# Kernel tuning notes

Measured on AMD Instinct MI355X. Metric: run time of the kernel, lower is better.

Reference implementation:

```python
import jax, jax.numpy as jnp
import numpy as np

VOCAB = 32000; DIM = 512; NL = 6; B = 2; L = 1024
DI = 2 * DIM      # d_inner (expand=2)
DS = 16           # d_state
DC = 4            # d_conv
DR = DIM // 16    # dt_rank = ceil(512/16) = 32


def setup_inputs() -> dict:
    key = jax.random.key(0)
    ks = jax.random.split(key, 10)
    s = 0.02
    tokens = jax.random.randint(ks[0], (B, L), 0, VOCAB)
    pos_emb = jax.random.normal(ks[1], (1, L, DIM)) * s
    embed = jax.random.normal(ks[2], (VOCAB, DIM)) * s
    lm_w = jax.random.normal(ks[3], (VOCAB, DIM)) * s
    lm_b = jnp.zeros((VOCAB,), jnp.float32)
    in_proj_w = jax.random.normal(ks[4], (NL, 2 * DI, DIM)) * s
    conv_w = jax.random.normal(ks[5], (NL, DI, DC)) * s
    conv_b = jnp.zeros((NL, DI), jnp.float32)
    x_proj_w = jax.random.normal(ks[6], (NL, DR + 2 * DS, DI)) * s
    dt_proj_w = jax.random.normal(ks[7], (NL, DI, DR)) * s
    dt_proj_b = jnp.broadcast_to(jnp.log(jnp.expm1(jnp.float32(0.01))), (NL, DI)).astype(jnp.float32)
    A_log = jnp.log(jnp.broadcast_to(jnp.arange(1, DS + 1, dtype=jnp.float32), (NL, DI, DS)))
    Dp = jnp.ones((NL, DI), jnp.float32)
    out_w = jax.random.normal(ks[8], (NL, DIM, DI)) * s
    ln_g = jnp.ones((NL, DIM), jnp.float32)
    ln_b = jnp.zeros((NL, DIM), jnp.float32)
    return dict(tokens=tokens, pos_emb=pos_emb, embed=embed, lm_w=lm_w, lm_b=lm_b,
                in_proj_w=in_proj_w, conv_w=conv_w, conv_b=conv_b, x_proj_w=x_proj_w,
                dt_proj_w=dt_proj_w, dt_proj_b=dt_proj_b, A_log=A_log, Dp=Dp,
                out_w=out_w, ln_g=ln_g, ln_b=ln_b)


def silu(x):
    return x * jax.nn.sigmoid(x)


def layernorm(x, g, b, eps=1e-5):
    mu = jnp.mean(x, -1, keepdims=True)
    var = jnp.var(x, -1, keepdims=True)
    return (x - mu) * jax.lax.rsqrt(var + eps) * g + b


def causal_dwconv(x, w, b):
    # x: (B,L,DI), w: (DI,DC) depthwise, left-pad causal
    xp = jnp.pad(x, ((0, 0), (DC - 1, 0), (0, 0)))
    y = b
    for k in range(DC):
        y = y + w[:, k] * xp[:, k:k + x.shape[1], :]
    return y


def selective_scan(u, dt, A, Bm, Cm, Dp):
    # u,dt: (B,L,DI); A: (DI,DS); Bm,Cm: (B,L,DS)
    dA = jnp.exp(dt[..., None] * A)                       # (B,L,DI,DS)
    dBu = dt[..., None] * Bm[:, :, None, :] * u[..., None]
    h0 = jnp.zeros((u.shape[0], DI, DS), u.dtype)

    def step(h, inp):
        dA_t, dBu_t, C_t = inp
        h = dA_t * h + dBu_t
        y = jnp.einsum('bdn,bn->bd', h, C_t)
        return h, y

    _, ys = jax.lax.scan(step, h0, (dA.transpose(1, 0, 2, 3),
                                    dBu.transpose(1, 0, 2, 3),
                                    Cm.transpose(1, 0, 2)))
    return ys.transpose(1, 0, 2) + u * Dp


def mamba_block(x, in_w, cw, cb, xp_w, dtw, dtb, A_log, Dp, ow):
    xz = jnp.einsum('bld,ed->ble', x, in_w)               # (B,L,2*DI)
    xc, z = jnp.split(xz, 2, axis=-1)
    xc = silu(causal_dwconv(xc, cw, cb))
    x_dbl = jnp.einsum('bld,ed->ble', xc, xp_w)           # (B,L,DR+2*DS)
    dt, Bm, Cm = jnp.split(x_dbl, [DR, DR + DS], axis=-1)
    dt = jax.nn.softplus(jnp.einsum('blr,dr->bld', dt, dtw) + dtb)
    A = -jnp.exp(A_log)
    y = selective_scan(xc, dt, A, Bm, Cm, Dp)
    y = y * silu(z)
    return jnp.einsum('bld,ed->ble', y, ow)


def reference(tokens, pos_emb, embed, lm_w, lm_b, in_proj_w, conv_w, conv_b,
              x_proj_w, dt_proj_w, dt_proj_b, A_log, Dp, out_w, ln_g, ln_b):
    x = embed[tokens] + pos_emb[:, :tokens.shape[1]]
    for i in range(NL):
        res = x
        x = mamba_block(x, in_proj_w[i], conv_w[i], conv_b[i], x_proj_w[i],
                        dt_proj_w[i], dt_proj_b[i], A_log[i], Dp[i], out_w[i])
        x = layernorm(x + res, ln_g[i], ln_b[i])
    return jnp.einsum('bld,vd->blv', x, lm_w) + lm_b
```

## Files before the change

kernel.cpp:

```cpp
#include <hip/hip_runtime.h>
#include <hip/hip_bf16.h>
#include <math.h>

#define BB 2
#define LL 1024
#define DIM 512
#define NL 6
#define DI 1024
#define DS 16
#define DC 4
#define DR 32
#define VOCAB 32000
#define M_ROWS (BB * LL)
#define CCH 64
#define CHLEN (LL / CCH)
#define KSPLIT 8

typedef unsigned short u16;
typedef __attribute__((ext_vector_type(8))) short bf16x8;
typedef __attribute__((ext_vector_type(4))) float f32x4;

__device__ __forceinline__ u16 f2bf(float f) {
    unsigned u = __float_as_uint(f);
    u += 0x7FFF + ((u >> 16) & 1);
    return (u16)(u >> 16);
}
#define SWZ(r, c) ((c) ^ (((r) >> 1) & 3))

__global__ __launch_bounds__(256) void cast_all(const float* __restrict__ lm,
                                                const float* __restrict__ inw,
                                                const float* __restrict__ ow,
                                                const float* __restrict__ xp,
                                                u16* __restrict__ lmb,
                                                u16* __restrict__ inb,
                                                u16* __restrict__ owb_,
                                                u16* __restrict__ xpb) {
    int idx = blockIdx.x * 256 + threadIdx.x;
    const float* src; u16* dst; int off;
    if (idx < 2048000)      { src = lm;  dst = lmb;  off = idx; }
    else if (idx < 2834432) { src = inw; dst = inb;  off = idx - 2048000; }
    else if (idx < 3227648) { src = ow;  dst = owb_; off = idx - 2834432; }
    else                    { src = xp;  dst = xpb;  off = idx - 3227648; }
    float4 v0 = ((const float4*)src)[off * 2];
    float4 v1 = ((const float4*)src)[off * 2 + 1];
    union { u16 h[8]; int4 v; } r;
    r.h[0] = f2bf(v0.x); r.h[1] = f2bf(v0.y); r.h[2] = f2bf(v0.z); r.h[3] = f2bf(v0.w);
    r.h[4] = f2bf(v1.x); r.h[5] = f2bf(v1.y); r.h[6] = f2bf(v1.z); r.h[7] = f2bf(v1.w);
    ((int4*)dst)[off] = r.v;
}

__global__ __launch_bounds__(256) void embed_kernel(const int* __restrict__ tok,
                                                    const float* __restrict__ pos,
                                                    const float* __restrict__ emb,
                                                    float* __restrict__ x,
                                                    u16* __restrict__ xb) {
    int idx = blockIdx.x * 256 + threadIdx.x;
    int d = idx & (DIM - 1);
    int l = (idx >> 9) & (LL - 1);
    int b = idx >> 19;
    int t = tok[b * LL + l];
    float v = emb[(size_t)t * DIM + d] + pos[l * DIM + d];
    x[idx] = v;
    xb[idx] = f2bf(v);
}

__global__ __launch_bounds__(256) void gemm_bf16(const u16* __restrict__ A,
                                                 const u16* __restrict__ W,
                                                 const float* __restrict__ bias,
                                                 float* __restrict__ C,
                                                 int M, int N, int K,
                                                 int lda, int ldw) {
    __shared__ __align__(16) u16 As[2 * 4096];
    __shared__ __align__(16) u16 Ws[2 * 4096];
    const int t = threadIdx.x;
    const int l = t & 63;
    const int w = t >> 6;
    const int nwg = gridDim.x;
    const int q = nwg >> 3, r8 = nwg & 7;
    const int xcd = blockIdx.x & 7, rank = blockIdx.x >> 3;
    const int wgid = (xcd < r8 ? xcd * (q + 1) : r8 * (q + 1) + (xcd - r8) * q) + rank;
    const int Mb = M >> 7;
    const int bm = (wgid % Mb) * 128;
    const int bn = (wgid / Mb) * 128;
    const int wm = (w >> 1) * 64;
    const int wn = (w & 1) * 64;

    f32x4 acc[4][4] = {};
    const int nt = K >> 5;

    auto STAGE = [&](int bufi, int k0) {
#pragma unroll
        for (int p = 0; p < 2; ++p) {
            const int i = (p * 4 + w) * 64 + l;
            const int row = i >> 2;
            const int kq = SWZ(row, i & 3);
            __builtin_amdgcn_global_load_lds(
                (const __attribute__((address_space(1))) unsigned int*)
                    (A + (size_t)(bm + row) * lda + k0 + kq * 8),
                (__attribute__((address_space(3))) unsigned int*)
                    (As + bufi * 4096 + (p * 4 + w) * 512),
                16, 0, 0);
            __builtin_amdgcn_global_load_lds(
                (const __attribute__((address_space(1))) unsigned int*)
                    (W + (size_t)(bn + row) * ldw + k0 + kq * 8),
                (__attribute__((address_space(3))) unsigned int*)
                    (Ws + bufi * 4096 + (p * 4 + w) * 512),
                16, 0, 0);
        }
    };
    auto COMPUTE = [&](int bufi) {
        const u16* Ab = As + bufi * 4096;
        const u16* Wb = Ws + bufi * 4096;
#pragma unroll
        for (int mi = 0; mi < 4; ++mi) {
            const int ar = wm + mi * 16 + (l & 15);
            bf16x8 a = *(const bf16x8*)(Ab + ar * 32 + SWZ(ar, l >> 4) * 8);
#pragma unroll
            for (int ni = 0; ni < 4; ++ni) {
                const int wr = wn + ni * 16 + (l & 15);
                bf16x8 b = *(const bf16x8*)(Wb + wr * 32 + SWZ(wr, l >> 4) * 8);
                acc[mi][ni] = __builtin_amdgcn_mfma_f32_16x16x32_bf16(b, a, acc[mi][ni], 0, 0, 0);
            }
        }
    };

    STAGE(0, 0);
    for (int tt = 0; tt < nt; ++tt) {
        if (tt + 1 < nt) {
            STAGE((tt + 1) & 1, (tt + 1) << 5);
            asm volatile("s_waitcnt vmcnt(4)\ns_barrier" ::: "memory");
        } else {
            asm volatile("s_waitcnt vmcnt(0)\ns_barrier" ::: "memory");
        }
        COMPUTE(tt & 1);
        asm volatile("s_waitcnt lgkmcnt(0)\ns_barrier" ::: "memory");
    }

#pragma unroll
    for (int mi = 0; mi < 4; ++mi) {
        const int row = bm + wm + mi * 16 + (l & 15);
#pragma unroll
        for (int ni = 0; ni < 4; ++ni) {
            const int col = bn + wn + ni * 16 + ((l >> 4) << 2);
            float4 v;
            v.x = acc[mi][ni][0]; v.y = acc[mi][ni][1];
            v.z = acc[mi][ni][2]; v.w = acc[mi][ni][3];
            if (bias != nullptr) {
                float4 b4 = *(const float4*)(bias + col);
                v.x += b4.x; v.y += b4.y; v.z += b4.z; v.w += b4.w;
            }
            *(float4*)(C + (size_t)row * N + col) = v;
        }
    }
}

__global__ __launch_bounds__(256) void gemm_n64(const u16* __restrict__ A,
                                                const u16* __restrict__ W,
                                                float* __restrict__ out,
                                                int lda, int ldw, int ldc,
                                                int KS, int pstride) {
    __shared__ __align__(16) u16 As[2 * 4096];
    __shared__ __align__(16) u16 Ws[2 * 2048];
    const int t = threadIdx.x;
    const int l = t & 63;
    const int w = t >> 6;
    const int kz = blockIdx.x;
    const int bm = blockIdx.y * 128;
    const int bnn = blockIdx.z * 64;
    const int wm = w * 32;

    f32x4 acc[2][4] = {};
    const int nt = KS >> 5;
    const int kbeg = kz * KS;

    auto STAGE = [&](int bufi, int k0) {
#pragma unroll
        for (int p = 0; p < 2; ++p) {
            const int i = p * 256 + w * 64 + l;
            const int row = i >> 2;
            const int kq = SWZ(row, i & 3);
            __builtin_amdgcn_global_load_lds(
                (const __attribute__((address_space(1))) unsigned int*)
                    (A + (size_t)(bm + row) * lda + k0 + kq * 8),
                (__attribute__((address_space(3))) unsigned int*)
                    (As + bufi * 4096 + (p * 256 + w * 64) * 8),
                16, 0, 0);
        }
        {
            const int i = w * 64 + l;
            const int row = i >> 2;
            const int kq = SWZ(row, i & 3);
            __builtin_amdgcn_global_load_lds(
                (const __attribute__((address_space(1))) unsigned int*)
                    (W + (size_t)(bnn + row) * ldw + k0 + kq * 8),
                (__attribute__((address_space(3))) unsigned int*)
                    (Ws + bufi * 2048 + (w * 64) * 8),
                16, 0, 0);
        }
    };
    auto COMPUTE = [&](int bufi) {
        const u16* Ab = As + bufi * 4096;
        const u16* Wb = Ws + bufi * 2048;
#pragma unroll
        for (int mi = 0; mi < 2; ++mi) {
            const int ar = wm + mi * 16 + (l & 15);
            bf16x8 a = *(const bf16x8*)(Ab + ar * 32 + SWZ(ar, l >> 4) * 8);
#pragma unroll
            for (int ni = 0; ni < 4; ++ni) {
                const int wr = ni * 16 + (l & 15);
                bf16x8 b = *(const bf16x8*)(Wb + wr * 32 + SWZ(wr, l >> 4) * 8);
                acc[mi][ni] = __builtin_amdgcn_mfma_f32_16x16x32_bf16(b, a, acc[mi][ni], 0, 0, 0);
            }
        }
    };

    STAGE(0, kbeg);
    for (int tt = 0; tt < nt; ++tt) {
        if (tt + 1 < nt) {
            STAGE((tt + 1) & 1, kbeg + ((tt + 1) << 5));
            asm volatile("s_waitcnt vmcnt(3)\ns_barrier" ::: "memory");
        } else {
            asm volatile("s_waitcnt vmcnt(0)\ns_barrier" ::: "memory");
        }
        COMPUTE(tt & 1);
        asm volatile("s_waitcnt lgkmcnt(0)\ns_barrier" ::: "memory");
    }

    float* op = out + (size_t)kz * pstride;
#pragma unroll
    for (int mi = 0; mi < 2; ++mi) {
        const int row = bm + wm + mi * 16 + (l & 15);
#pragma unroll
        for (int ni = 0; ni < 4; ++ni) {
            const int col = bnn + ni * 16 + ((l >> 4) << 2);
            float4 v;
            v.x = acc[mi][ni][0]; v.y = acc[mi][ni][1];
            v.z = acc[mi][ni][2]; v.w = acc[mi][ni][3];
            *(float4*)(op + (size_t)row * ldc + col) = v;
        }
    }
}

__global__ __launch_bounds__(256) void xdred_dt(const float* __restrict__ Pf,
                                                const float* __restrict__ dtw,
                                                const float* __restrict__ dtb,
                                                float* __restrict__ xd,
                                                float* __restrict__ dt) {
    __shared__ float xds[64];
    const int m = blockIdx.x;
    const int t = threadIdx.x;
    if (t < 64) {
        float s = 0.f;
#pragma unroll
        for (int kz = 0; kz < KSPLIT; ++kz)
            s += Pf[(size_t)kz * (M_ROWS * 64) + m * 64 + t];
        xds[t] = s;
        xd[m * 64 + t] = s;
    }
    __syncthreads();
    const int d0 = t * 4;
    const float4 bv = *(const float4*)(dtb + d0);
    float a0 = bv.x, a1 = bv.y, a2 = bv.z, a3 = bv.w;
    const float* w0p = dtw + (size_t)(d0 + 0) * DR;
    const float* w1p = dtw + (size_t)(d0 + 1) * DR;
    const float* w2p = dtw + (size_t)(d0 + 2) * DR;
    const float* w3p = dtw + (size_t)(d0 + 3) * DR;
#pragma unroll
    for (int k = 0; k < DR; k += 4) {
        float4 xv = *(const float4*)&xds[k];
        float4 w0 = *(const float4*)(w0p + k);
        float4 w1 = *(const float4*)(w1p + k);
        float4 w2 = *(const float4*)(w2p + k);
        float4 w3 = *(const float4*)(w3p + k);
        a0 += w0.x * xv.x + w0.y * xv.y + w0.z * xv.z + w0.w * xv.w;
        a1 += w1.x * xv.x + w1.y * xv.y + w1.z * xv.z + w1.w * xv.w;
        a2 += w2.x * xv.x + w2.y * xv.y + w2.z * xv.z + w2.w * xv.w;
        a3 += w3.x * xv.x + w3.y * xv.y + w3.z * xv.z + w3.w * xv.w;
    }
    a0 = (a0 > 20.f) ? a0 : log1pf(__expf(a0));
    a1 = (a1 > 20.f) ? a1 : log1pf(__expf(a1));
    a2 = (a2 > 20.f) ? a2 : log1pf(__expf(a2));
    a3 = (a3 > 20.f) ? a3 : log1pf(__expf(a3));
    float4 v; v.x = a0; v.y = a1; v.z = a2; v.w = a3;
    *(float4*)(dt + (size_t)m * DI + d0) = v;
}

__global__ __launch_bounds__(256) void conv_silu(const float* __restrict__ xz,
                                                 const float* __restrict__ cw,
                                                 const float* __restrict__ cb,
                                                 float* __restrict__ xc,
                                                 u16* __restrict__ xcb) {
    int idx = blockIdx.x * 256 + threadIdx.x;
    int c = idx & (DI - 1);
    int l = (idx >> 10) & (LL - 1);
    int b = idx >> 20;
    float acc = cb[c];
#pragma unroll
    for (int k = 0; k < DC; ++k) {
        int ll = l + k - (DC - 1);
        if (ll >= 0)
            acc += cw[c * DC + k] * xz[((size_t)(b * LL + ll)) * (2 * DI) + c];
    }
    float v = acc / (1.f + __expf(-acc));
    xc[idx] = v;
    xcb[idx] = f2bf(v);
}

__global__ __launch_bounds__(256) void scan_pass1(const float* __restrict__ xc,
                                                  const float* __restrict__ dt,
                                                  const float* __restrict__ xdbl,
                                                  const float* __restrict__ A_log,
                                                  float* __restrict__ S,
                                                  float* __restrict__ Q) {
    const int d = blockIdx.x * 256 + threadIdx.x;
    const int b = blockIdx.y;
    const int c = blockIdx.z;
    float a[DS];
#pragma unroll
    for (int q = 0; q < 4; ++q) {
        float4 al = *(const float4*)(A_log + d * DS + q * 4);
        a[q * 4 + 0] = -__expf(al.x);
        a[q * 4 + 1] = -__expf(al.y);
        a[q * 4 + 2] = -__expf(al.z);
        a[q * 4 + 3] = -__expf(al.w);
    }
    float Qr[DS];
#pragma unroll
    for (int n = 0; n < DS; ++n) Qr[n] = 0.f;
    float Ssum = 0.f;

    const int l0 = c * CHLEN;
    const float* dtp = dt + ((size_t)b * LL + l0) * DI + d;
    const float* up  = xc + ((size_t)b * LL + l0) * DI + d;
    const float* xdp = xdbl + ((size_t)b * LL + l0) * 64 + DR;

    for (int l = 0; l < CHLEN; ++l) {
        float dtv = dtp[(size_t)l * DI];
        float uv  = up[(size_t)l * DI];
        float wv = dtv * uv;
        Ssum += dtv;
#pragma unroll
        for (int q = 0; q < 4; ++q) {
            float4 Bv = *(const float4*)(xdp + l * 64 + q * 4);
            float dA0 = __expf(dtv * a[q * 4 + 0]);
            float dA1 = __expf(dtv * a[q * 4 + 1]);
            float dA2 = __expf(dtv * a[q * 4 + 2]);
            float dA3 = __expf(dtv * a[q * 4 + 3]);
            Qr[q * 4 + 0] = dA0 * Qr[q * 4 + 0] + wv * Bv.x;
            Qr[q * 4 + 1] = dA1 * Qr[q * 4 + 1] + wv * Bv.y;
            Qr[q * 4 + 2] = dA2 * Qr[q * 4 + 2] + wv * Bv.z;
            Qr[q * 4 + 3] = dA3 * Qr[q * 4 + 3] + wv * Bv.w;
        }
    }
    S[((size_t)b * CCH + c) * DI + d] = Ssum;
    float* Qp = Q + (((size_t)b * CCH + c) * DI + d) * DS;
#pragma unroll
    for (int q = 0; q < 4; ++q) {
        float4 o;
        o.x = Qr[q * 4 + 0]; o.y = Qr[q * 4 + 1];
        o.z = Qr[q * 4 + 2]; o.w = Qr[q * 4 + 3];
        *(float4*)(Qp + q * 4) = o;
    }
}

__global__ __launch_bounds__(256) void scan_pass2(const float* __restrict__ A_log,
                                                  const float* __restrict__ S,
                                                  float* __restrict__ Q) {
    const int idx = blockIdx.x * 256 + threadIdx.x;
    const int b = idx >> 14;
    const int dn = idx & 16383;
    const int d = dn >> 4;
    const float a = -__expf(A_log[dn]);
    float h = 0.f;
    for (int c = 0; c < CCH; ++c) {
        const size_t soff = ((size_t)b * CCH + c) * DI + d;
        const size_t qoff = ((size_t)b * CCH + c) * (size_t)(DI * DS) + dn;
        float P = __expf(a * S[soff]);
        float qv = Q[qoff];
        Q[qoff] = h;
        h = P * h + qv;
    }
}

__global__ __launch_bounds__(256) void scan_pass3(const float* __restrict__ xc,
                                                  const float* __restrict__ dt,
                                                  const float* __restrict__ xdbl,
                                                  const float* __restrict__ xz,
                                                  const float* __restrict__ A_log,
                                                  const float* __restrict__ Dpp,
                                                  const float* __restrict__ Q,
                                                  u16* __restrict__ y) {
    const int d = blockIdx.x * 256 + threadIdx.x;
    const int b = blockIdx.y;
    const int c = blockIdx.z;
    float a[DS];
#pragma unroll
    for (int q = 0; q < 4; ++q) {
        float4 al = *(const float4*)(A_log + d * DS + q * 4);
        a[q * 4 + 0] = -__expf(al.x);
        a[q * 4 + 1] = -__expf(al.y);
        a[q * 4 + 2] = -__expf(al.z);
        a[q * 4 + 3] = -__expf(al.w);
    }
    float h[DS];
    const float* Qp = Q + (((size_t)b * CCH + c) * DI + d) * DS;
#pragma unroll
    for (int q = 0; q < 4; ++q) {
        float4 hv = *(const float4*)(Qp + q * 4);
        h[q * 4 + 0] = hv.x; h[q * 4 + 1] = hv.y;
        h[q * 4 + 2] = hv.z; h[q * 4 + 3] = hv.w;
    }
    const float dp = Dpp[d];

    const int l0 = c * CHLEN;
    const float* dtp = dt + ((size_t)b * LL + l0) * DI + d;
    const float* up  = xc + ((size_t)b * LL + l0) * DI + d;
    const float* xdp = xdbl + ((size_t)b * LL + l0) * 64 + DR;
    const float* zp  = xz + ((size_t)b * LL + l0) * (2 * DI) + DI + d;
    u16* yp = y + ((size_t)b * LL + l0) * DI + d;

    for (int l = 0; l < CHLEN; ++l) {
        float dtv = dtp[(size_t)l * DI];
        float uv  = up[(size_t)l * DI];
        float wv = dtv * uv;
        float p = 0.f;
#pragma unroll
        for (int q = 0; q < 4; ++q) {
            float4 Bv = *(const float4*)(xdp + l * 64 + q * 4);
            float4 Cv = *(const float4*)(xdp + l * 64 + 16 + q * 4);
            float dA0 = __expf(dtv * a[q * 4 + 0]);
            float dA1 = __expf(dtv * a[q * 4 + 1]);
            float dA2 = __expf(dtv * a[q * 4 + 2]);
            float dA3 = __expf(dtv * a[q * 4 + 3]);
            h[q * 4 + 0] = dA0 * h[q * 4 + 0] + wv * Bv.x;
            h[q * 4 + 1] = dA1 * h[q * 4 + 1] + wv * Bv.y;
            h[q * 4 + 2] = dA2 * h[q * 4 + 2] + wv * Bv.z;
            h[q * 4 + 3] = dA3 * h[q * 4 + 3] + wv * Bv.w;
            p += h[q * 4 + 0] * Cv.x + h[q * 4 + 1] * Cv.y +
                 h[q * 4 + 2] * Cv.z + h[q * 4 + 3] * Cv.w;
        }
        float zv = zp[(size_t)l * (2 * DI)];
        float g = zv / (1.f + __expf(-zv));
        yp[(size_t)l * DI] = f2bf((p + uv * dp) * g);
    }
}

__global__ __launch_bounds__(256) void add_ln(const float* __restrict__ o,
                                              float* __restrict__ x,
                                              const float* __restrict__ g,
                                              const float* __restrict__ b,
                                              u16* __restrict__ xb) {
    int m = blockIdx.x;
    int t = threadIdx.x;
    const float* xr = x + (size_t)m * DIM;
    const float* orr = o + (size_t)m * DIM;
    float v0 = xr[t] + orr[t];
    float v1 = xr[t + 256] + orr[t + 256];
    float s = v0 + v1;
    float ss = v0 * v0 + v1 * v1;
#pragma unroll
    for (int off = 32; off > 0; off >>= 1) {
        s += __shfl_down(s, off, 64);
        ss += __shfl_down(ss, off, 64);
    }
    __shared__ float sb[4], ssb[4];
    int w = t >> 6;
    if ((t & 63) == 0) { sb[w] = s; ssb[w] = ss; }
    __syncthreads();
    float stot = sb[0] + sb[1] + sb[2] + sb[3];
    float sstot = ssb[0] + ssb[1] + ssb[2] + ssb[3];
    float mean = stot * (1.f / DIM);
    float var = sstot * (1.f / DIM) - mean * mean;
    float rs = rsqrtf(var + 1e-5f);
    float* xw = x + (size_t)m * DIM;
    float o0 = (v0 - mean) * rs * g[t] + b[t];
    float o1 = (v1 - mean) * rs * g[t + 256] + b[t + 256];
    xw[t] = o0;
    xw[t + 256] = o1;
    xb[(size_t)m * DIM + t] = f2bf(o0);
    xb[(size_t)m * DIM + t + 256] = f2bf(o1);
}

extern "C" void kernel_launch(void* const* d_in, const int* in_sizes, int n_in,
                              void* d_out, int out_size, void* d_ws, size_t ws_size,
                              hipStream_t stream) {
    const int*   tokens = (const int*)d_in[0];
    const float* pos    = (const float*)d_in[1];
    const float* emb    = (const float*)d_in[2];
    const float* lm_w   = (const float*)d_in[3];
    const float* lm_b   = (const float*)d_in[4];
    const float* in_w   = (const float*)d_in[5];
    const float* cw     = (const float*)d_in[6];
    const float* cb     = (const float*)d_in[7];
    const float* xpw    = (const float*)d_in[8];
    const float* dtw    = (const float*)d_in[9];
    const float* dtb    = (const float*)d_in[10];
    const float* A_log  = (const float*)d_in[11];
    const float* Dpp    = (const float*)d_in[12];
    const float* ow     = (const float*)d_in[13];
    const float* lng    = (const float*)d_in[14];
    const float* lnb    = (const float*)d_in[15];
    float* out = (float*)d_out;

    float* ws = (float*)d_ws;
    float* x    = ws;
    float* xz   = x + 1048576;
    float* xc   = xz + 4194304;
    float* xd   = xc + 2097152;
    float* dt   = xd + 131072;
    float* o    = dt + 2097152;
    float* S    = o + 1048576;
    float* Qb   = S + 131072;
    float* Pf   = Qb + 2097152;
    u16* xb     = (u16*)(Pf + 1048576);
    u16* yb     = xb + 1048576;
    u16* xcb    = yb + 2097152;
    u16* lm_wb  = xcb + 2097152;
    u16* in_wb  = lm_wb + 16384000;
    u16* owb    = in_wb + 6291456;
    u16* xpwb   = owb + 3145728;

    cast_all<<<12800, 256, 0, stream>>>(lm_w, in_w, ow, xpw,
                                        lm_wb, in_wb, owb, xpwb);

    embed_kernel<<<M_ROWS * DIM / 256, 256, 0, stream>>>(tokens, pos, emb, x, xb);

    for (int i = 0; i < NL; ++i) {
        gemm_bf16<<<(2048 / 128) * (M_ROWS / 128), 256, 0, stream>>>(
            xb, in_wb + (size_t)i * 2048 * 512, nullptr, xz,
            M_ROWS, 2048, 512, 512, 512);
        conv_silu<<<M_ROWS * DI / 256, 256, 0, stream>>>(
            xz, cw + (size_t)i * DI * DC, cb + (size_t)i * DI, xc, xcb);
        gemm_n64<<<dim3(KSPLIT, M_ROWS / 128, 1), 256, 0, stream>>>(
            xcb, xpwb + (size_t)i * 64 * 1024, Pf,
            1024, 1024, 64, 1024 / KSPLIT, M_ROWS * 64);
        xdred_dt<<<M_ROWS, 256, 0, stream>>>(
            Pf, dtw + (size_t)i * DI * DR, dtb + (size_t)i * DI, xd, dt);
        scan_pass1<<<dim3(DI / 256, BB, CCH), 256, 0, stream>>>(
            xc, dt, xd, A_log + (size_t)i * DI * DS, S, Qb);
        scan_pass2<<<(BB * DI * DS) / 256, 256, 0, stream>>>(
            A_log + (size_t)i * DI * DS, S, Qb);
        scan_pass3<<<dim3(DI / 256, BB, CCH), 256, 0, stream>>>(
            xc, dt, xd, xz, A_log + (size_t)i * DI * DS, Dpp + (size_t)i * DI, Qb, yb);
        gemm_n64<<<dim3(1, M_ROWS / 128, 512 / 64), 256, 0, stream>>>(
            yb, owb + (size_t)i * 512 * 1024, o,
            1024, 1024, 512, 1024, 0);
        add_ln<<<M_ROWS, 256, 0, stream>>>(
            o, x, lng + (size_t)i * DIM, lnb + (size_t)i * DIM, xb);
    }

    gemm_bf16<<<(VOCAB / 128) * (M_ROWS / 128), 256, 0, stream>>>(
        xb, lm_wb, lm_b, out, M_ROWS, VOCAB, 512, 512, 512);
}
```

Before: 888.4 us.

## Store in_proj output as bf16, split-K out_proj, and shrink scan_pass2 blocks

The in_proj GEMM now runs through gemm_n64 with a bf16 epilogue, so conv_silu and scan_pass3 read xz as bf16 instead of fp32. This halves the traffic for the largest per-layer intermediate. The out_proj GEMM is split four ways along K, giving more blocks in flight, and add_ln sums the four partial results. scan_pass2 moves to 64-thread blocks to launch more blocks. The trade-off is reduced precision on z and the conv input, plus extra partial-sum traffic for out_proj.

```diff
diff --git a/kernel.cpp b/kernel.cpp
--- a/kernel.cpp
+++ b/kernel.cpp
@@ -15,6 +15,7 @@
 #define CCH 64
 #define CHLEN (LL / CCH)
 #define KSPLIT 8
+#define OSPLIT 4
 
 typedef unsigned short u16;
 typedef __attribute__((ext_vector_type(8))) short bf16x8;
@@ -24,6 +25,9 @@
     unsigned u = __float_as_uint(f);
     u += 0x7FFF + ((u >> 16) & 1);
     return (u16)(u >> 16);
+}
+__device__ __forceinline__ float bf2f(u16 h) {
+    return __uint_as_float(((unsigned)h) << 16);
 }
 #define SWZ(r, c) ((c) ^ (((r) >> 1) & 3))
 
@@ -157,6 +161,7 @@
 __global__ __launch_bounds__(256) void gemm_n64(const u16* __restrict__ A,
                                                 const u16* __restrict__ W,
                                                 float* __restrict__ out,
+                                                u16* __restrict__ outb,
                                                 int lda, int ldw, int ldc,
                                                 int KS, int pstride) {
     __shared__ __align__(16) u16 As[2 * 4096];
@@ -226,17 +231,33 @@
         asm volatile("s_waitcnt lgkmcnt(0)\ns_barrier" ::: "memory");
     }
 
-    float* op = out + (size_t)kz * pstride;
-#pragma unroll
-    for (int mi = 0; mi < 2; ++mi) {
-        const int row = bm + wm + mi * 16 + (l & 15);
-#pragma unroll
-        for (int ni = 0; ni < 4; ++ni) {
-            const int col = bnn + ni * 16 + ((l >> 4) << 2);
-            float4 v;
-            v.x = acc[mi][ni][0]; v.y = acc[mi][ni][1];
-            v.z = acc[mi][ni][2]; v.w = acc[mi][ni][3];
-            *(float4*)(op + (size_t)row * ldc + col) = v;
+    if (outb != nullptr) {
+        u16* opb = outb + (size_t)kz * pstride;
+#pragma unroll
+        for (int mi = 0; mi < 2; ++mi) {
+            const int row = bm + wm + mi * 16 + (l & 15);
+#pragma unroll
+            for (int ni = 0; ni < 4; ++ni) {
+                const int col = bnn + ni * 16 + ((l >> 4) << 2);
+                ushort4 v;
+                v.x = f2bf(acc[mi][ni][0]); v.y = f2bf(acc[mi][ni][1]);
+                v.z = f2bf(acc[mi][ni][2]); v.w = f2bf(acc[mi][ni][3]);
+                *(ushort4*)(opb + (size_t)row * ldc + col) = v;
+            }
+        }
+    } else {
+        float* op = out + (size_t)kz * pstride;
+#pragma unroll
+        for (int mi = 0; mi < 2; ++mi) {
+            const int row = bm + wm + mi * 16 + (l & 15);
+#pragma unroll
+            for (int ni = 0; ni < 4; ++ni) {
+                const int col = bnn + ni * 16 + ((l >> 4) << 2);
+                float4 v;
+                v.x = acc[mi][ni][0]; v.y = acc[mi][ni][1];
+                v.z = acc[mi][ni][2]; v.w = acc[mi][ni][3];
+                *(float4*)(op + (size_t)row * ldc + col) = v;
+            }
         }
     }
 }
@@ -285,7 +306,7 @@
     *(float4*)(dt + (size_t)m * DI + d0) = v;
 }
 
-__global__ __launch_bounds__(256) void conv_silu(const float* __restrict__ xz,
+__global__ __launch_bounds__(256) void conv_silu(const u16* __restrict__ xzb,
                                                  const float* __restrict__ cw,
                                                  const float* __restrict__ cb,
                                                  float* __restrict__ xc,
@@ -299,7 +320,7 @@
     for (int k = 0; k < DC; ++k) {
         int ll = l + k - (DC - 1);
         if (ll >= 0)
-            acc += cw[c * DC + k] * xz[((size_t)(b * LL + ll)) * (2 * DI) + c];
+            acc += cw[c * DC + k] * bf2f(xzb[((size_t)(b * LL + ll)) * (2 * DI) + c]);
     }
     float v = acc / (1.f + __expf(-acc));
     xc[idx] = v;
@@ -363,10 +384,10 @@
     }
 }
 
-__global__ __launch_bounds__(256) void scan_pass2(const float* __restrict__ A_log,
-                                                  const float* __restrict__ S,
-                                                  float* __restrict__ Q) {
-    const int idx = blockIdx.x * 256 + threadIdx.x;
+__global__ __launch_bounds__(64) void scan_pass2(const float* __restrict__ A_log,
+                                                 const float* __restrict__ S,
+                                                 float* __restrict__ Q) {
+    const int idx = blockIdx.x * 64 + threadIdx.x;
     const int b = idx >> 14;
     const int dn = idx & 16383;
     const int d = dn >> 4;
@@ -385,7 +406,7 @@
 __global__ __launch_bounds__(256) void scan_pass3(const float* __restrict__ xc,
                                                   const float* __restrict__ dt,
                                                   const float* __restrict__ xdbl,
-                                                  const float* __restrict__ xz,
+                                                  const u16* __restrict__ xzb,
                                                   const float* __restrict__ A_log,
                                                   const float* __restrict__ Dpp,
                                                   const float* __restrict__ Q,
@@ -416,7 +437,7 @@
     const float* dtp = dt + ((size_t)b * LL + l0) * DI + d;
     const float* up  = xc + ((size_t)b * LL + l0) * DI + d;
     const float* xdp = xdbl + ((size_t)b * LL + l0) * 64 + DR;
-    const float* zp  = xz + ((size_t)b * LL + l0) * (2 * DI) + DI + d;
+    const u16* zp = xzb + ((size_t)b * LL + l0) * (2 * DI) + DI + d;
     u16* yp = y + ((size_t)b * LL + l0) * DI + d;
 
     for (int l = 0; l < CHLEN; ++l) {
@@ -439,23 +460,29 @@
             p += h[q * 4 + 0] * Cv.x + h[q * 4 + 1] * Cv.y +
                  h[q * 4 + 2] * Cv.z + h[q * 4 + 3] * Cv.w;
         }
-        float zv = zp[(size_t)l * (2 * DI)];
+        float zv = bf2f(zp[(size_t)l * (2 * DI)]);
         float g = zv / (1.f + __expf(-zv));
         yp[(size_t)l * DI] = f2bf((p + uv * dp) * g);
     }
 }
 
-__global__ __launch_bounds__(256) void add_ln(const float* __restrict__ o,
+__global__ __launch_bounds__(256) void add_ln(const float* __restrict__ opart,
                                               float* __restrict__ x,
                                               const float* __restrict__ g,
                                               const float* __restrict__ b,
                                               u16* __restrict__ xb) {
+    const int PS = M_ROWS * DIM;
     int m = blockIdx.x;
     int t = threadIdx.x;
     const float* xr = x + (size_t)m * DIM;
-    const float* orr = o + (size_t)m * DIM;
-    float v0 = xr[t] + orr[t];
-    float v1 = xr[t + 256] + orr[t + 256];
+    float v0 = xr[t];
+    float v1 = xr[t + 256];
+#pragma unroll
+    for (int kz = 0; kz < OSPLIT; ++kz) {
+        const float* op = opart + (size_t)kz * PS + (size_t)m * DIM;
+        v0 += op[t];
+        v1 += op[t + 256];
+    }
     float s = v0 + v1;
     float ss = v0 * v0 + v1 * v1;
 #pragma unroll
@@ -504,15 +531,15 @@
 
     float* ws = (float*)d_ws;
     float* x    = ws;
-    float* xz   = x + 1048576;
-    float* xc   = xz + 4194304;
+    float* xc   = x + 1048576;
     float* xd   = xc + 2097152;
     float* dt   = xd + 131072;
-    float* o    = dt + 2097152;
-    float* S    = o + 1048576;
+    float* S    = dt + 2097152;
     float* Qb   = S + 131072;
     float* Pf   = Qb + 2097152;
-    u16* xb     = (u16*)(Pf + 1048576);
+    float* Pf2  = Pf + 1048576;
+    u16* xzb    = (u16*)(Pf2 + 4194304);
+    u16* xb     = xzb + 4194304;
     u16* yb     = xb + 1048576;
     u16* xcb    = yb + 2097152;
     u16* lm_wb  = xcb + 2097152;
@@ -526,27 +553,27 @@
     embed_kernel<<<M_ROWS * DIM / 256, 256, 0, stream>>>(tokens, pos, emb, x, xb);
 
     for (int i = 0; i < NL; ++i) {
-        gemm_bf16<<<(2048 / 128) * (M_ROWS / 128), 256, 0, stream>>>(
-            xb, in_wb + (size_t)i * 2048 * 512, nullptr, xz,
-            M_ROWS, 2048, 512, 512, 512);
+        gemm_n64<<<dim3(1, M_ROWS / 128, 2048 / 64), 256, 0, stream>>>(
+            xb, in_wb + (size_t)i * 2048 * 512, nullptr, xzb,
+            512, 512, 2048, 512, 0);
         conv_silu<<<M_ROWS * DI / 256, 256, 0, stream>>>(
-            xz, cw + (size_t)i * DI * DC, cb + (size_t)i * DI, xc, xcb);
+            xzb, cw + (size_t)i * DI * DC, cb + (size_t)i * DI, xc, xcb);
         gemm_n64<<<dim3(KSPLIT, M_ROWS / 128, 1), 256, 0, stream>>>(
-            xcb, xpwb + (size_t)i * 64 * 1024, Pf,
+            xcb, xpwb + (size_t)i * 64 * 1024, Pf, nullptr,
             1024, 1024, 64, 1024 / KSPLIT, M_ROWS * 64);
         xdred_dt<<<M_ROWS, 256, 0, stream>>>(
             Pf, dtw + (size_t)i * DI * DR, dtb + (size_t)i * DI, xd, dt);
         scan_pass1<<<dim3(DI / 256, BB, CCH), 256, 0, stream>>>(
             xc, dt, xd, A_log + (size_t)i * DI * DS, S, Qb);
-        scan_pass2<<<(BB * DI * DS) / 256, 256, 0, stream>>>(
+        scan_pass2<<<(BB * DI * DS) / 64, 64, 0, stream>>>(
             A_log + (size_t)i * DI * DS, S, Qb);
         scan_pass3<<<dim3(DI / 256, BB, CCH), 256, 0, stream>>>(
-            xc, dt, xd, xz, A_log + (size_t)i * DI * DS, Dpp + (size_t)i * DI, Qb, yb);
-        gemm_n64<<<dim3(1, M_ROWS / 128, 512 / 64), 256, 0, stream>>>(
-            yb, owb + (size_t)i * 512 * 1024, o,
-            1024, 1024, 512, 1024, 0);
+            xc, dt, xd, xzb, A_log + (size_t)i * DI * DS, Dpp + (size_t)i * DI, Qb, yb);
+        gemm_n64<<<dim3(OSPLIT, M_ROWS / 128, 512 / 64), 256, 0, stream>>>(
+            yb, owb + (size_t)i * 512 * 1024, Pf2, nullptr,
+            1024, 1024, 512, 1024 / OSPLIT, M_ROWS * 512);
         add_ln<<<M_ROWS, 256, 0, stream>>>(
-            o, x, lng + (size_t)i * DIM, lnb + (size_t)i * DIM, xb);
+            Pf2, x, lng + (size_t)i * DIM, lnb + (size_t)i * DIM, xb);
     }
 
     gemm_bf16<<<(VOCAB / 128) * (M_ROWS / 128), 256, 0, stream>>>(
```

Measured after the change: 838.1 us. -5.7%, faster.
